# Performance work log

Measured on AMD Instinct MI355X. Metric: run time of the kernel, lower is better.

## Reference

```python
import jax, jax.numpy as jnp
import numpy as np

B, NQ, NV, DIM, HEADS, K = 2, 2048, 2048, 256, 8, 8
HD = DIM // HEADS
HID = 4 * DIM
SCALE = HD ** -0.5
EPS = 1e-5


def setup_inputs() -> dict:
    key = jax.random.key(0)
    ks = jax.random.split(key, 40)
    r = lambda i, s: jax.random.normal(ks[i], s, jnp.float32) * 0.02
    inp = {
        'q': jax.random.normal(ks[0], (B, NQ, DIM), jnp.float32),
        'v': jax.random.normal(ks[1], (B, NV, DIM), jnp.float32),
        'q_pos': jax.random.normal(ks[2], (B, NQ, 3), jnp.float32),
        'v_pos': jax.random.normal(ks[3], (B, NV, 3), jnp.float32),
        'self_knn_index': jax.random.randint(ks[4], (B, NQ, K), 0, NQ, jnp.int32),
        'cross_knn_index': jax.random.randint(ks[5], (B, NQ, K), 0, NV, jnp.int32),
        # LayerNorms (gamma=1, beta=0)
        'norm1_g': jnp.ones(DIM), 'norm1_b': jnp.zeros(DIM),
        'normq_g': jnp.ones(DIM), 'normq_b': jnp.zeros(DIM),
        'normv_g': jnp.ones(DIM), 'normv_b': jnp.zeros(DIM),
        'norm2_g': jnp.ones(DIM), 'norm2_b': jnp.zeros(DIM),
        # self-attention (qkv_bias=False), proj has bias
        'sa_qkv_w': r(6, (DIM, 3 * DIM)),
        'sa_proj_w': r(7, (DIM, DIM)), 'sa_proj_b': jnp.zeros(DIM),
        # cross-attention: q proj and kv proj (no bias), out proj with bias
        'ca_q_w': r(8, (DIM, DIM)),
        'ca_kv_w': r(9, (DIM, 2 * DIM)),
        'ca_proj_w': r(10, (DIM, DIM)), 'ca_proj_b': jnp.zeros(DIM),
        # MLP
        'fc1_w': r(11, (DIM, HID)), 'fc1_b': jnp.zeros(HID),
        'fc2_w': r(12, (HID, DIM)), 'fc2_b': jnp.zeros(DIM),
        # kNN maps
        'knn_w': r(13, (2 * DIM, DIM)), 'knn_b': jnp.zeros(DIM),
        'merge_w': r(14, (2 * DIM, DIM)), 'merge_b': jnp.zeros(DIM),
        'knnx_w': r(15, (2 * DIM, DIM)), 'knnx_b': jnp.zeros(DIM),
        'mergex_w': r(16, (2 * DIM, DIM)), 'mergex_b': jnp.zeros(DIM),
    }
    return inp


def _ln(x, g, b):
    m = x.mean(-1, keepdims=True)
    var = x.var(-1, keepdims=True)
    return (x - m) / jnp.sqrt(var + EPS) * g + b


def _heads(x):  # [B,N,DIM] -> [B,H,N,HD]
    Bx, N, _ = x.shape
    return x.reshape(Bx, N, HEADS, HD).transpose(0, 2, 1, 3)


def _attend(qh, kh, vh, proj_w, proj_b):
    a = jax.nn.softmax(jnp.einsum('bhqd,bhkd->bhqk', qh, kh) * SCALE, axis=-1)
    o = jnp.einsum('bhqk,bhkd->bhqd', a, vh)
    Bx, _, N, _ = o.shape
    o = o.transpose(0, 2, 1, 3).reshape(Bx, N, DIM)
    return o @ proj_w + proj_b


_gather = jax.vmap(lambda pts, idx: pts[idx])  # ([N,D],[Nq,K]) -> [Nq,K,D]


def _knn_feature(qn, vn, idx):  # gather -> diff/cat -> [B,Nq,K,2D]
    local = _gather(vn, idx)                      # [B,Nq,K,D]
    qe = qn[:, :, None, :]                        # [B,Nq,1,D]
    return jnp.concatenate([local - qe, jnp.broadcast_to(qe, local.shape)], -1)


def reference(q, v, q_pos, v_pos, self_knn_index, cross_knn_index,
              norm1_g, norm1_b, normq_g, normq_b, normv_g, normv_b,
              norm2_g, norm2_b, sa_qkv_w, sa_proj_w, sa_proj_b,
              ca_q_w, ca_kv_w, ca_proj_w, ca_proj_b,
              fc1_w, fc1_b, fc2_w, fc2_b,
              knn_w, knn_b, merge_w, merge_b,
              knnx_w, knnx_b, mergex_w, mergex_b):
    # ---- self-attention block with self-kNN branch ----
    nq = _ln(q, norm1_g, norm1_b)
    qkv = nq @ sa_qkv_w
    qh, kh, vh = (_heads(t) for t in jnp.split(qkv, 3, axis=-1))
    sa_out = _attend(qh, kh, vh, sa_proj_w, sa_proj_b)
    f = _knn_feature(nq, nq, self_knn_index)
    knn_out = jax.nn.leaky_relu(f @ knn_w + knn_b, 0.2).max(axis=-2)
    q1 = jnp.concatenate([sa_out, knn_out], -1) @ merge_w + merge_b
    q = q + q1
    # ---- cross-attention block with cross-kNN branch ----
    nq2 = _ln(q, normq_g, normq_b)
    nv = _ln(v, normv_g, normv_b)
    qh = _heads(nq2 @ ca_q_w)
    kh, vh = (_heads(t) for t in jnp.split(nv @ ca_kv_w, 2, axis=-1))
    ca_out = _attend(qh, kh, vh, ca_proj_w, ca_proj_b)
    f = _knn_feature(nq2, nv, cross_knn_index)
    knnx_out = jax.nn.leaky_relu(f @ knnx_w + knnx_b, 0.2).max(axis=-2)
    q2 = jnp.concatenate([ca_out, knnx_out], -1) @ mergex_w + mergex_b
    q = q + q2
    # ---- MLP block ----
    h = _ln(q, norm2_g, norm2_b)
    h = jax.nn.gelu(h @ fc1_w + fc1_b, approximate=False)
    q = q + (h @ fc2_w + fc2_b)
    return q
```

## Files before the change

kernel.cpp:

```cpp
#include <hip/hip_runtime.h>
#include <math.h>

#define NQC   2048
#define NKVC  2048
#define DIMC  256
#define SCALEF 0.17677669529663687f

typedef short bfrag __attribute__((ext_vector_type(8)));
typedef float ffrag __attribute__((ext_vector_type(4)));
typedef unsigned short us8 __attribute__((ext_vector_type(8)));

__device__ __forceinline__ float gelu_exact(float x) {
    return 0.5f * x * (1.0f + erff(x * 0.70710678118654752f));
}
__device__ __forceinline__ unsigned short f2bf(float f) {
    union { float f; unsigned u; } v; v.f = f;
    unsigned r = v.u + 0x7FFFu + ((v.u >> 16) & 1u);
    return (unsigned short)(r >> 16);
}
__device__ __forceinline__ float bf2f(unsigned short u) {
    union { unsigned u; float f; } v; v.u = ((unsigned)u) << 16;
    return v.f;
}

__device__ __forceinline__ void ln_row(
    const float* __restrict__ x, const float* __restrict__ g,
    const float* __restrict__ b, unsigned short* __restrict__ y, int row)
{
    int lane = threadIdx.x & 63;
    const float* xr = x + (size_t)row * DIMC + lane * 4;
    float4 vv = *(const float4*)xr;
    float s  = vv.x + vv.y + vv.z + vv.w;
    float sq = vv.x*vv.x + vv.y*vv.y + vv.z*vv.z + vv.w*vv.w;
    #pragma unroll
    for (int off = 32; off >= 1; off >>= 1) {
        s  += __shfl_xor(s, off);
        sq += __shfl_xor(sq, off);
    }
    float mean = s * (1.0f/DIMC);
    float inv  = rsqrtf(sq * (1.0f/DIMC) - mean*mean + 1e-5f);
    float4 gg = *(const float4*)(g + lane*4);
    float4 bb = *(const float4*)(b + lane*4);
    ushort4 o;
    o.x = f2bf((vv.x - mean) * inv * gg.x + bb.x);
    o.y = f2bf((vv.y - mean) * inv * gg.y + bb.y);
    o.z = f2bf((vv.z - mean) * inv * gg.z + bb.z);
    o.w = f2bf((vv.w - mean) * inv * gg.w + bb.w);
    *(ushort4*)(y + (size_t)row * DIMC + lane * 4) = o;
}

__global__ __launch_bounds__(256) void prep_ln(
    const float* __restrict__ qkv, const float* __restrict__ knn,
    const float* __restrict__ proj, const float* __restrict__ merge,
    const float* __restrict__ caq, const float* __restrict__ knnx,
    const float* __restrict__ cakv, const float* __restrict__ projx,
    const float* __restrict__ mergex, const float* __restrict__ fc1,
    const float* __restrict__ fc2, unsigned short* __restrict__ dst,
    const float* __restrict__ lx, const float* __restrict__ lg,
    const float* __restrict__ lb, unsigned short* __restrict__ ly)
{
    if (blockIdx.x >= 1536) {
        int row = (blockIdx.x - 1536) * 4 + (threadIdx.x >> 6);
        ln_row(lx, lg, lb, ly, row);
        return;
    }
    int e = (blockIdx.x * 256 + threadIdx.x) * 4;
    float v[4];
    float scale = 1.0f;
    if (e < 327680) {
        int n = e >> 8, k = e & 255;
        if (n < 768) {
            const float* s = qkv + (size_t)k * 768 + n;
            #pragma unroll
            for (int i = 0; i < 4; ++i) v[i] = s[(size_t)i * 768];
            if (n < 256) scale = SCALEF;
        } else if (n < 1024) {
            const float* s = knn + (size_t)k * 256 + (n - 768);
            #pragma unroll
            for (int i = 0; i < 4; ++i) v[i] = s[(size_t)i * 256];
        } else {
            const float* s = knn + (size_t)k * 256 + (n - 1024);
            #pragma unroll
            for (int i = 0; i < 4; ++i) v[i] = s[65536 + (size_t)i * 256] - s[(size_t)i * 256];
        }
    } else if (e < 393216) {
        int l = e - 327680, n = l >> 8, k = l & 255;
        const float* s = proj + (size_t)k * 256 + n;
        #pragma unroll
        for (int i = 0; i < 4; ++i) v[i] = s[(size_t)i * 256];
    } else if (e < 524288) {
        int l = e - 393216, n = l >> 9, k = l & 511;
        const float* s = merge + (size_t)k * 256 + n;
        #pragma unroll
        for (int i = 0; i < 4; ++i) v[i] = s[(size_t)i * 256];
    } else if (e < 655360) {
        int l = e - 524288, n = l >> 8, k = l & 255;
        if (n < 256) {
            const float* s = caq + (size_t)k * 256 + n;
            #pragma unroll
            for (int i = 0; i < 4; ++i) v[i] = s[(size_t)i * 256];
            scale = SCALEF;
        } else {
            const float* s = knnx + (size_t)k * 256 + (n - 256);
            #pragma unroll
            for (int i = 0; i < 4; ++i) v[i] = s[65536 + (size_t)i * 256] - s[(size_t)i * 256];
        }
    } else if (e < 851968) {
        int l = e - 655360, n = l >> 8, k = l & 255;
        if (n < 512) {
            const float* s = cakv + (size_t)k * 512 + n;
            #pragma unroll
            for (int i = 0; i < 4; ++i) v[i] = s[(size_t)i * 512];
        } else {
            const float* s = knnx + (size_t)k * 256 + (n - 512);
            #pragma unroll
            for (int i = 0; i < 4; ++i) v[i] = s[(size_t)i * 256];
        }
    } else if (e < 917504) {
        int l = e - 851968, n = l >> 8, k = l & 255;
        const float* s = projx + (size_t)k * 256 + n;
        #pragma unroll
        for (int i = 0; i < 4; ++i) v[i] = s[(size_t)i * 256];
    } else if (e < 1048576) {
        int l = e - 917504, n = l >> 9, k = l & 511;
        const float* s = mergex + (size_t)k * 256 + n;
        #pragma unroll
        for (int i = 0; i < 4; ++i) v[i] = s[(size_t)i * 256];
    } else if (e < 1310720) {
        int l = e - 1048576, n = l >> 8, k = l & 255;
        const float* s = fc1 + (size_t)k * 1024 + n;
        #pragma unroll
        for (int i = 0; i < 4; ++i) v[i] = s[(size_t)i * 1024];
    } else {
        int l = e - 1310720, n = l >> 10, k = l & 1023;
        const float* s = fc2 + (size_t)k * 256 + n;
        #pragma unroll
        for (int i = 0; i < 4; ++i) v[i] = s[(size_t)i * 256];
    }
    ushort4 o;
    o.x = f2bf(v[0] * scale); o.y = f2bf(v[1] * scale);
    o.z = f2bf(v[2] * scale); o.w = f2bf(v[3] * scale);
    *(ushort4*)(dst + e) = o;
}

__global__ __launch_bounds__(256) void ln2_b(
    const float* __restrict__ x1, const float* __restrict__ g1,
    const float* __restrict__ b1, unsigned short* __restrict__ y1,
    const float* __restrict__ x2, const float* __restrict__ g2,
    const float* __restrict__ b2, unsigned short* __restrict__ y2)
{
    int wid = threadIdx.x >> 6;
    int blk = blockIdx.x;
    if (blk < 1024) ln_row(x1, g1, b1, y1, blk * 4 + wid);
    else            ln_row(x2, g2, b2, y2, (blk - 1024) * 4 + wid);
}

__global__ __launch_bounds__(256) void ln_b(
    const float* __restrict__ x, const float* __restrict__ g,
    const float* __restrict__ b, unsigned short* __restrict__ y)
{
    ln_row(x, g, b, y, blockIdx.x * 4 + (threadIdx.x >> 6));
}

template<int ACT, int RESID, int OUTBF>
__global__ __launch_bounds__(256) void gemm64(
    const unsigned short* __restrict__ A, int lda,
    const unsigned short* __restrict__ Wt,
    const float* __restrict__ bias,
    const float* __restrict__ resid, int ldr,
    void* __restrict__ Cp, int ldc, int Kc)
{
    __shared__ unsigned short Alds[64][72];
    __shared__ unsigned short Wlds[64][72];
    const int tid = threadIdx.x;
    const int wid = tid >> 6, lane = tid & 63;
    const int lm = lane & 15, quad = lane >> 4;
    const int wr = wid >> 1, wc = wid & 1;
    const int row0 = blockIdx.y * 64, col0 = blockIdx.x * 64;
    const int ar = tid >> 2, ac = (tid & 3) * 16;
    const unsigned short* Ag = A  + (size_t)(row0 + ar) * lda + ac;
    const unsigned short* Wg = Wt + (size_t)(col0 + ar) * Kc  + ac;

    us8 a0 = *(const us8*)Ag;
    us8 a1 = *(const us8*)(Ag + 8);
    us8 w0 = *(const us8*)Wg;
    us8 w1 = *(const us8*)(Wg + 8);

    ffrag acc[2][2];
    #pragma unroll
    for (int mi = 0; mi < 2; ++mi)
        #pragma unroll
        for (int ni = 0; ni < 2; ++ni)
            acc[mi][ni] = (ffrag){0.f, 0.f, 0.f, 0.f};

    for (int k0 = 0;;) {
        __syncthreads();
        *(us8*)&Alds[ar][ac]   = a0;
        *(us8*)&Alds[ar][ac+8] = a1;
        *(us8*)&Wlds[ar][ac]   = w0;
        *(us8*)&Wlds[ar][ac+8] = w1;
        __syncthreads();
        k0 += 64;
        if (k0 < Kc) {
            a0 = *(const us8*)(Ag + k0);
            a1 = *(const us8*)(Ag + k0 + 8);
            w0 = *(const us8*)(Wg + k0);
            w1 = *(const us8*)(Wg + k0 + 8);
        }
        #pragma unroll
        for (int kc = 0; kc < 2; ++kc) {
            bfrag af[2], bw[2];
            #pragma unroll
            for (int mi = 0; mi < 2; ++mi)
                af[mi] = *(const bfrag*)&Alds[wr*32 + mi*16 + lm][kc*32 + quad*8];
            #pragma unroll
            for (int ni = 0; ni < 2; ++ni)
                bw[ni] = *(const bfrag*)&Wlds[wc*32 + ni*16 + lm][kc*32 + quad*8];
            #pragma unroll
            for (int mi = 0; mi < 2; ++mi)
                #pragma unroll
                for (int ni = 0; ni < 2; ++ni)
                    acc[mi][ni] = __builtin_amdgcn_mfma_f32_16x16x32_bf16(
                        af[mi], bw[ni], acc[mi][ni], 0, 0, 0);
        }
        if (k0 >= Kc) break;
    }
    #pragma unroll
    for (int mi = 0; mi < 2; ++mi) {
        #pragma unroll
        for (int ni = 0; ni < 2; ++ni) {
            int gr = row0 + wr*32 + mi*16 + quad*4;
            int gc = col0 + wc*32 + ni*16 + lm;
            float bv = bias ? bias[gc] : 0.f;
            #pragma unroll
            for (int r = 0; r < 4; ++r) {
                float o = acc[mi][ni][r] + bv;
                if (ACT == 1) o = gelu_exact(o);
                if (RESID) o += resid[(size_t)(gr + r) * ldr + gc];
                if (OUTBF) ((unsigned short*)Cp)[(size_t)(gr + r) * ldc + gc] = f2bf(o);
                else       ((float*)Cp)[(size_t)(gr + r) * ldc + gc] = o;
            }
        }
    }
}

template<int ACT, int RESID, int OUTBF>
__global__ __launch_bounds__(512) void gemm64x8(
    const unsigned short* __restrict__ A, int lda,
    const unsigned short* __restrict__ Wt,
    const float* __restrict__ bias,
    const float* __restrict__ resid, int ldr,
    void* __restrict__ Cp, int ldc, int Kc)
{
    __shared__ unsigned short Alds[2][64][72];
    __shared__ unsigned short Wlds[2][64][72];
    __shared__ float Red[64][68];
    const int tid = threadIdx.x;
    const int g = tid >> 8;
    const int t = tid & 255;
    const int wid2 = (tid >> 6) & 3, lane = tid & 63;
    const int lm = lane & 15, quad = lane >> 4;
    const int wr = wid2 >> 1, wc = wid2 & 1;
    const int row0 = blockIdx.y * 64, col0 = blockIdx.x * 64;
    const int ar = t >> 2, ac = (t & 3) * 16;
    const int KH = Kc >> 1;
    const unsigned short* Ag = A  + (size_t)(row0 + ar) * lda + g * KH + ac;
    const unsigned short* Wg = Wt + (size_t)(col0 + ar) * Kc  + g * KH + ac;

    us8 a0 = *(const us8*)Ag;
    us8 a1 = *(const us8*)(Ag + 8);
    us8 w0 = *(const us8*)Wg;
    us8 w1 = *(const us8*)(Wg + 8);

    ffrag acc[2][2];
    #pragma unroll
    for (int mi = 0; mi < 2; ++mi)
        #pragma unroll
        for (int ni = 0; ni < 2; ++ni)
            acc[mi][ni] = (ffrag){0.f, 0.f, 0.f, 0.f};

    for (int k0 = 0;;) {
        __syncthreads();
        *(us8*)&Alds[g][ar][ac]   = a0;
        *(us8*)&Alds[g][ar][ac+8] = a1;
        *(us8*)&Wlds[g][ar][ac]   = w0;
        *(us8*)&Wlds[g][ar][ac+8] = w1;
        __syncthreads();
        k0 += 64;
        if (k0 < KH) {
            a0 = *(const us8*)(Ag + k0);
            a1 = *(const us8*)(Ag + k0 + 8);
            w0 = *(const us8*)(Wg + k0);
            w1 = *(const us8*)(Wg + k0 + 8);
        }
        #pragma unroll
        for (int kc = 0; kc < 2; ++kc) {
            bfrag af[2], bw[2];
            #pragma unroll
            for (int mi = 0; mi < 2; ++mi)
                af[mi] = *(const bfrag*)&Alds[g][wr*32 + mi*16 + lm][kc*32 + quad*8];
            #pragma unroll
            for (int ni = 0; ni < 2; ++ni)
                bw[ni] = *(const bfrag*)&Wlds[g][wc*32 + ni*16 + lm][kc*32 + quad*8];
            #pragma unroll
            for (int mi = 0; mi < 2; ++mi)
                #pragma unroll
                for (int ni = 0; ni < 2; ++ni)
                    acc[mi][ni] = __builtin_amdgcn_mfma_f32_16x16x32_bf16(
                        af[mi], bw[ni], acc[mi][ni], 0, 0, 0);
        }
        if (k0 >= KH) break;
    }
    __syncthreads();
    if (g == 1) {
        #pragma unroll
        for (int mi = 0; mi < 2; ++mi)
            #pragma unroll
            for (int ni = 0; ni < 2; ++ni) {
                int lr = wr*32 + mi*16 + quad*4;
                int lc = wc*32 + ni*16 + lm;
                #pragma unroll
                for (int r = 0; r < 4; ++r)
                    Red[lr + r][lc] = acc[mi][ni][r];
            }
    }
    __syncthreads();
    if (g == 0) {
        #pragma unroll
        for (int mi = 0; mi < 2; ++mi) {
            #pragma unroll
            for (int ni = 0; ni < 2; ++ni) {
                int lr = wr*32 + mi*16 + quad*4;
                int lc = wc*32 + ni*16 + lm;
                int gr = row0 + lr;
                int gc = col0 + lc;
                float bv = bias ? bias[gc] : 0.f;
                #pragma unroll
                for (int r = 0; r < 4; ++r) {
                    float o = acc[mi][ni][r] + Red[lr + r][lc] + bv;
                    if (ACT == 1) o = gelu_exact(o);
                    if (RESID) o += resid[(size_t)(gr + r) * ldr + gc];
                    if (OUTBF) ((unsigned short*)Cp)[(size_t)(gr + r) * ldc + gc] = f2bf(o);
                    else       ((float*)Cp)[(size_t)(gr + r) * ldc + gc] = o;
                }
            }
        }
    }
}

__global__ __launch_bounds__(256) void gemm64_dual(
    const unsigned short* __restrict__ XB,
    const unsigned short* __restrict__ NVB,
    const unsigned short* __restrict__ WT2,
    const unsigned short* __restrict__ WT3,
    unsigned short* __restrict__ A2,
    unsigned short* __restrict__ A3)
{
    const unsigned short* A; const unsigned short* Wt;
    unsigned short* C; int ldc, col0;
    if (blockIdx.x < 8) { A = XB;  Wt = WT2; C = A2; ldc = 512; col0 = blockIdx.x * 64; }
    else                { A = NVB; Wt = WT3; C = A3; ldc = 768; col0 = (blockIdx.x - 8) * 64; }

    __shared__ unsigned short Alds[64][72];
    __shared__ unsigned short Wlds[64][72];
    const int tid = threadIdx.x;
    const int wid = tid >> 6, lane = tid & 63;
    const int lm = lane & 15, quad = lane >> 4;
    const int wr = wid >> 1, wc = wid & 1;
    const int row0 = blockIdx.y * 64;
    const int ar = tid >> 2, ac = (tid & 3) * 16;
    const unsigned short* Ag = A  + (size_t)(row0 + ar) * 256 + ac;
    const unsigned short* Wg = Wt + (size_t)(col0 + ar) * 256 + ac;

    us8 a0 = *(const us8*)Ag;
    us8 a1 = *(const us8*)(Ag + 8);
    us8 w0 = *(const us8*)Wg;
    us8 w1 = *(const us8*)(Wg + 8);

    ffrag acc[2][2];
    #pragma unroll
    for (int mi = 0; mi < 2; ++mi)
        #pragma unroll
        for (int ni = 0; ni < 2; ++ni)
            acc[mi][ni] = (ffrag){0.f, 0.f, 0.f, 0.f};

    for (int k0 = 0;;) {
        __syncthreads();
        *(us8*)&Alds[ar][ac]   = a0;
        *(us8*)&Alds[ar][ac+8] = a1;
        *(us8*)&Wlds[ar][ac]   = w0;
        *(us8*)&Wlds[ar][ac+8] = w1;
        __syncthreads();
        k0 += 64;
        if (k0 < 256) {
            a0 = *(const us8*)(Ag + k0);
            a1 = *(const us8*)(Ag + k0 + 8);
            w0 = *(const us8*)(Wg + k0);
            w1 = *(const us8*)(Wg + k0 + 8);
        }
        #pragma unroll
        for (int kc = 0; kc < 2; ++kc) {
            bfrag af[2], bw[2];
            #pragma unroll
            for (int mi = 0; mi < 2; ++mi)
                af[mi] = *(const bfrag*)&Alds[wr*32 + mi*16 + lm][kc*32 + quad*8];
            #pragma unroll
            for (int ni = 0; ni < 2; ++ni)
                bw[ni] = *(const bfrag*)&Wlds[wc*32 + ni*16 + lm][kc*32 + quad*8];
            #pragma unroll
            for (int mi = 0; mi < 2; ++mi)
                #pragma unroll
                for (int ni = 0; ni < 2; ++ni)
                    acc[mi][ni] = __builtin_amdgcn_mfma_f32_16x16x32_bf16(
                        af[mi], bw[ni], acc[mi][ni], 0, 0, 0);
        }
        if (k0 >= 256) break;
    }
    #pragma unroll
    for (int mi = 0; mi < 2; ++mi) {
        #pragma unroll
        for (int ni = 0; ni < 2; ++ni) {
            int gr = row0 + wr*32 + mi*16 + quad*4;
            int gc = col0 + wc*32 + ni*16 + lm;
            #pragma unroll
            for (int r = 0; r < 4; ++r)
                C[(size_t)(gr + r) * ldc + gc] = f2bf(acc[mi][ni][r]);
        }
    }
}

__global__ __launch_bounds__(256) void gemm64_comb(
    const unsigned short* __restrict__ Op, const float* __restrict__ Lp,
    const unsigned short* __restrict__ Wt,
    const float* __restrict__ bias,
    unsigned short* __restrict__ C, int ldc)
{
    __shared__ unsigned short Alds[64][72];
    __shared__ unsigned short Wlds[64][72];
    const int tid = threadIdx.x;
    const int wid = tid >> 6, lane = tid & 63;
    const int lm = lane & 15, quad = lane >> 4;
    const int wr = wid >> 1, wc = wid & 1;
    const int row0 = blockIdx.y * 64, col0 = blockIdx.x * 64;
    const int ar = tid >> 2, ac = (tid & 3) * 16;
    const int grow = row0 + ar;
    const unsigned short* O0 = Op + (size_t)grow * 256 + ac;
    const unsigned short* O1 = Op + (size_t)(4096 + grow) * 256 + ac;
    const float* L0 = Lp + (size_t)grow * 8;
    const float* L1 = Lp + (size_t)(4096 + grow) * 8;
    const unsigned short* Wg = Wt + (size_t)(col0 + ar) * 256 + ac;

    us8 o00 = *(const us8*)O0;
    us8 o01 = *(const us8*)(O0 + 8);
    us8 o10 = *(const us8*)O1;
    us8 o11 = *(const us8*)(O1 + 8);
    float li = 1.0f / (L0[ac >> 5] + L1[ac >> 5]);
    us8 w0 = *(const us8*)Wg;
    us8 w1 = *(const us8*)(Wg + 8);

    ffrag acc[2][2];
    #pragma unroll
    for (int mi = 0; mi < 2; ++mi)
        #pragma unroll
        for (int ni = 0; ni < 2; ++ni)
            acc[mi][ni] = (ffrag){0.f, 0.f, 0.f, 0.f};

    for (int k0 = 0;;) {
        us8 ac0, ac1;
        #pragma unroll
        for (int i = 0; i < 8; ++i) {
            ac0[i] = f2bf((bf2f(o00[i]) + bf2f(o10[i])) * li);
            ac1[i] = f2bf((bf2f(o01[i]) + bf2f(o11[i])) * li);
        }
        __syncthreads();
        *(us8*)&Alds[ar][ac]   = ac0;
        *(us8*)&Alds[ar][ac+8] = ac1;
        *(us8*)&Wlds[ar][ac]   = w0;
        *(us8*)&Wlds[ar][ac+8] = w1;
        __syncthreads();
        k0 += 64;
        if (k0 < 256) {
            o00 = *(const us8*)(O0 + k0);
            o01 = *(const us8*)(O0 + k0 + 8);
            o10 = *(const us8*)(O1 + k0);
            o11 = *(const us8*)(O1 + k0 + 8);
            li = 1.0f / (L0[(k0 + ac) >> 5] + L1[(k0 + ac) >> 5]);
            w0 = *(const us8*)(Wg + k0);
            w1 = *(const us8*)(Wg + k0 + 8);
        }
        #pragma unroll
        for (int kc = 0; kc < 2; ++kc) {
            bfrag af[2], bw[2];
            #pragma unroll
            for (int mi = 0; mi < 2; ++mi)
                af[mi] = *(const bfrag*)&Alds[wr*32 + mi*16 + lm][kc*32 + quad*8];
            #pragma unroll
            for (int ni = 0; ni < 2; ++ni)
                bw[ni] = *(const bfrag*)&Wlds[wc*32 + ni*16 + lm][kc*32 + quad*8];
            #pragma unroll
            for (int mi = 0; mi < 2; ++mi)
                #pragma unroll
                for (int ni = 0; ni < 2; ++ni)
                    acc[mi][ni] = __builtin_amdgcn_mfma_f32_16x16x32_bf16(
                        af[mi], bw[ni], acc[mi][ni], 0, 0, 0);
        }
        if (k0 >= 256) break;
    }
    #pragma unroll
    for (int mi = 0; mi < 2; ++mi) {
        #pragma unroll
        for (int ni = 0; ni < 2; ++ni) {
            int gr = row0 + wr*32 + mi*16 + quad*4;
            int gc = col0 + wc*32 + ni*16 + lm;
            float bv = bias[gc];
            #pragma unroll
            for (int r = 0; r < 4; ++r)
                C[(size_t)(gr + r) * ldc + gc] = f2bf(acc[mi][ni][r] + bv);
        }
    }
}

__global__ __launch_bounds__(256) void attn_gather(
    const unsigned short* __restrict__ Qp, int ldq,
    const unsigned short* __restrict__ Kp, int ldk,
    const unsigned short* __restrict__ Vp, int ldv,
    unsigned short* __restrict__ Op, float* __restrict__ Lp,
    const unsigned short* __restrict__ P, int ldp,
    const unsigned short* __restrict__ Base, int ldb,
    const float* __restrict__ gbias, const int* __restrict__ idx,
    unsigned short* __restrict__ gout, int ldgo)
{
    __shared__ unsigned short Klds[64][40];
    __shared__ unsigned short Vt[32][72];
    __shared__ unsigned short Plds[4][16][72];
    int tid = threadIdx.x, wid = tid >> 6, lane = tid & 63;

    if (blockIdx.z >= 4) {
        int gbid = blockIdx.x + 32 * (blockIdx.y + 8 * (blockIdx.z - 4));
        int q = gbid * 4 + wid;
        int b = q >> 11;
        int c = lane * 4;
        ushort4 bu = *(const ushort4*)(Base + (size_t)q * ldb + c);
        float4 bi = *(const float4*)(gbias + c);
        float bsx = bf2f(bu.x) + bi.x, bsy = bf2f(bu.y) + bi.y;
        float bsz = bf2f(bu.z) + bi.z, bsw = bf2f(bu.w) + bi.w;
        float4 acc = make_float4(-3e38f, -3e38f, -3e38f, -3e38f);
        const int* ip = idx + (size_t)q * 8;
        #pragma unroll
        for (int k = 0; k < 8; ++k) {
            int j = ip[k];
            ushort4 pu = *(const ushort4*)(P + ((size_t)(b * NKVC + j)) * ldp + c);
            float t;
            t = bsx + bf2f(pu.x); t = t > 0.f ? t : 0.2f * t; acc.x = fmaxf(acc.x, t);
            t = bsy + bf2f(pu.y); t = t > 0.f ? t : 0.2f * t; acc.y = fmaxf(acc.y, t);
            t = bsz + bf2f(pu.z); t = t > 0.f ? t : 0.2f * t; acc.z = fmaxf(acc.z, t);
            t = bsw + bf2f(pu.w); t = t > 0.f ? t : 0.2f * t; acc.w = fmaxf(acc.w, t);
        }
        ushort4 o;
        o.x = f2bf(acc.x); o.y = f2bf(acc.y); o.z = f2bf(acc.z); o.w = f2bf(acc.w);
        *(ushort4*)(gout + (size_t)q * ldgo + c) = o;
        return;
    }

    int zc = blockIdx.z, bb = zc >> 1, ck = zc & 1;
    int h = blockIdx.y;
    int hoff = h * 32;
    int lm = lane & 15, quad = lane >> 4;
    size_t qbase  = (size_t)bb * NQC;
    size_t kvbase = (size_t)bb * NKVC;
    int q0 = blockIdx.x * 64 + wid * 16;

    bfrag aq = *(const bfrag*)(Qp + (qbase + q0 + lm) * (size_t)ldq + hoff + quad * 8);

    float l_r[4] = {0.f, 0.f, 0.f, 0.f};
    ffrag oacc[2];
    oacc[0] = (ffrag){0.f, 0.f, 0.f, 0.f};
    oacc[1] = (ffrag){0.f, 0.f, 0.f, 0.f};

    const int kkey = tid >> 2, kd0 = (tid & 3) * 8;
    const int vkey = tid & 63, vd0 = (tid >> 6) * 8;
    const unsigned short* kg0 = Kp + (kvbase + kkey) * (size_t)ldk + hoff + kd0;
    const unsigned short* vg0 = Vp + (kvbase + vkey) * (size_t)ldv + hoff + vd0;

    for (int kt = ck * 16; kt < ck * 16 + 16; ++kt) {
        us8 kv = *(const us8*)(kg0 + (size_t)kt * 64 * ldk);
        us8 vv = *(const us8*)(vg0 + (size_t)kt * 64 * ldv);
        __syncthreads();
        *(us8*)&Klds[kkey][kd0] = kv;
        #pragma unroll
        for (int i = 0; i < 8; ++i) Vt[vd0 + i][vkey] = vv[i];
        __syncthreads();

        ffrag sacc[4];
        #pragma unroll
        for (int t = 0; t < 4; ++t) {
            bfrag bk = *(const bfrag*)&Klds[t*16 + lm][quad * 8];
            sacc[t] = __builtin_amdgcn_mfma_f32_16x16x32_bf16(
                aq, bk, (ffrag){0.f,0.f,0.f,0.f}, 0, 0, 0);
        }

        #pragma unroll
        for (int r = 0; r < 4; ++r) {
            float p0 = __expf(sacc[0][r]), p1 = __expf(sacc[1][r]);
            float p2 = __expf(sacc[2][r]), p3 = __expf(sacc[3][r]);
            l_r[r] += (p0 + p1) + (p2 + p3);
            int row = quad * 4 + r;
            Plds[wid][row][lm +  0] = f2bf(p0);
            Plds[wid][row][lm + 16] = f2bf(p1);
            Plds[wid][row][lm + 32] = f2bf(p2);
            Plds[wid][row][lm + 48] = f2bf(p3);
        }
        asm volatile("s_waitcnt lgkmcnt(0)" ::: "memory");

        #pragma unroll
        for (int kc = 0; kc < 2; ++kc) {
            bfrag ap = *(const bfrag*)&Plds[wid][lm][kc*32 + quad*8];
            #pragma unroll
            for (int nt = 0; nt < 2; ++nt) {
                bfrag bv = *(const bfrag*)&Vt[nt*16 + lm][kc*32 + quad*8];
                oacc[nt] = __builtin_amdgcn_mfma_f32_16x16x32_bf16(
                    ap, bv, oacc[nt], 0, 0, 0);
            }
        }
    }
    #pragma unroll
    for (int nt = 0; nt < 2; ++nt)
        #pragma unroll
        for (int r = 0; r < 4; ++r)
            Op[((size_t)ck * 4096 + qbase + q0 + quad*4 + r) * 256 + hoff + nt*16 + lm]
                = f2bf(oacc[nt][r]);
    #pragma unroll
    for (int r = 0; r < 4; ++r) {
        float l = l_r[r];
        l += __shfl_xor(l, 1);
        l += __shfl_xor(l, 2);
        l += __shfl_xor(l, 4);
        l += __shfl_xor(l, 8);
        if (lm == 0)
            Lp[((size_t)ck * 4096 + qbase + q0 + quad*4 + r) * 8 + h] = l;
    }
}

extern "C" void kernel_launch(void* const* d_in, const int* in_sizes, int n_in,
                              void* d_out, int out_size, void* d_ws, size_t ws_size,
                              hipStream_t stream) {
    const float* q_in   = (const float*)d_in[0];
    const float* v_in   = (const float*)d_in[1];
    const int*   idx_s  = (const int*)d_in[4];
    const int*   idx_x  = (const int*)d_in[5];
    const float* n1g = (const float*)d_in[6],  *n1b = (const float*)d_in[7];
    const float* nqg = (const float*)d_in[8],  *nqb = (const float*)d_in[9];
    const float* nvg = (const float*)d_in[10], *nvb = (const float*)d_in[11];
    const float* n2g = (const float*)d_in[12], *n2b = (const float*)d_in[13];
    const float* sa_qkv_w  = (const float*)d_in[14];
    const float* sa_proj_w = (const float*)d_in[15];
    const float* sa_proj_b = (const float*)d_in[16];
    const float* ca_q_w    = (const float*)d_in[17];
    const float* ca_kv_w   = (const float*)d_in[18];
    const float* ca_proj_w = (const float*)d_in[19];
    const float* ca_proj_b = (const float*)d_in[20];
    const float* fc1_w = (const float*)d_in[21], *fc1_b = (const float*)d_in[22];
    const float* fc2_w = (const float*)d_in[23], *fc2_b = (const float*)d_in[24];
    const float* knn_w   = (const float*)d_in[25], *knn_b   = (const float*)d_in[26];
    const float* merge_w = (const float*)d_in[27], *merge_b = (const float*)d_in[28];
    const float* knnx_w  = (const float*)d_in[29], *knnx_b  = (const float*)d_in[30];
    const float* mergex_w = (const float*)d_in[31], *mergex_b = (const float*)d_in[32];
    float* out = (float*)d_out;

    unsigned short* A1      = (unsigned short*)d_ws;
    unsigned short* A2      = A1;
    unsigned short* A3      = A1 + (size_t)4096 * 512;
    unsigned short* Hb      = A1;
    unsigned short* KN      = A1 + (size_t)4096 * 1280;
    unsigned short* CC      = KN;
    unsigned short* XB      = CC + (size_t)4096 * 512;
    unsigned short* NVB     = XB + (size_t)4096 * 256;
    unsigned short* WT      = NVB + (size_t)4096 * 256;
    unsigned short* WT1     = WT;
    unsigned short* WTproj  = WT + 327680;
    unsigned short* WTmerge = WT + 393216;
    unsigned short* WT2     = WT + 524288;
    unsigned short* WT3     = WT + 655360;
    unsigned short* WTprojx = WT + 851968;
    unsigned short* WTmergex= WT + 917504;
    unsigned short* WTfc1   = WT + 1048576;
    unsigned short* WTfc2   = WT + 1310720;
    unsigned short* Opart   = WT + 1572864;
    float* Lpart = (float*)(Opart + (size_t)2 * 4096 * 256);

    dim3 blk(256), blk8(512);
    dim3 gAG(NQC / 64, 8, 8);

    prep_ln<<<dim3(2560), blk, 0, stream>>>(sa_qkv_w, knn_w, sa_proj_w, merge_w,
        ca_q_w, knnx_w, ca_kv_w, ca_proj_w, mergex_w, fc1_w, fc2_w, WT,
        q_in, n1g, n1b, XB);

    gemm64<0,0,1><<<dim3(20,64), blk, 0, stream>>>(XB, 256, WT1,
        nullptr, nullptr, 0, A1, 1280, 256);
    attn_gather<<<gAG, blk, 0, stream>>>(A1, 1280, A1+256, 1280, A1+512, 1280,
        Opart, Lpart, A1+768, 1280, A1+1024, 1280, knn_b, idx_s, CC+256, 512);
    gemm64_comb<<<dim3(4,64), blk, 0, stream>>>(Opart, Lpart, WTproj,
        sa_proj_b, CC, 512);
    gemm64x8<0,1,0><<<dim3(4,64), blk8, 0, stream>>>(CC, 512, WTmerge,
        merge_b, q_in, 256, out, 256, 512);

    ln2_b<<<dim3(2048), blk, 0, stream>>>(out, nqg, nqb, XB,
        v_in, nvg, nvb, NVB);
    gemm64_dual<<<dim3(20,64), blk, 0, stream>>>(XB, NVB, WT2, WT3, A2, A3);
    attn_gather<<<gAG, blk, 0, stream>>>(A2, 512, A3, 768, A3+256, 768,
        Opart, Lpart, A3+512, 768, A2+256, 512, knnx_b, idx_x, CC+256, 512);
    gemm64_comb<<<dim3(4,64), blk, 0, stream>>>(Opart, Lpart, WTprojx,
        ca_proj_b, CC, 512);
    gemm64x8<0,1,0><<<dim3(4,64), blk8, 0, stream>>>(CC, 512, WTmergex,
        mergex_b, out, 256, out, 256, 512);

    ln_b<<<dim3(1024), blk, 0, stream>>>(out, n2g, n2b, XB);
    gemm64<1,0,1><<<dim3(16,64), blk, 0, stream>>>(XB, 256, WTfc1,
        fc1_b, nullptr, 0, Hb, 1024, 256);
    gemm64x8<0,1,0><<<dim3(4,64), blk8, 0, stream>>>(Hb, 1024, WTfc2,
        fc2_b, out, 256, out, 256, 1024);
}
```

Before: 258.9 us.

## Fold attention output projection into merge weights and fuse combine with merge GEMM

Precomputes the product of proj_w and the attention half of merge_w, plus a folded bias, inside the prep and QKV kernels. The separate combine/proj GEMM and merge GEMM are replaced by one split-K kernel that normalises the partial attention outputs and multiplies them and the kNN branch concurrently. The v LayerNorm moves into the prep kernel. Softmax switches to a raw exp2 with log2e folded into the scale, and P is packed with a bf16 pack instruction through a permuted V layout. Intermediate rounding changes: the folded weights are rounded to bf16 and the attention output skips a rounding step.

```diff
diff --git a/kernel.cpp b/kernel.cpp
--- a/kernel.cpp
+++ b/kernel.cpp
@@ -4,7 +4,7 @@
 #define NQC   2048
 #define NKVC  2048
 #define DIMC  256
-#define SCALEF 0.17677669529663687f
+#define SCALEF 0.2550348810731232f
 
 typedef short bfrag __attribute__((ext_vector_type(8)));
 typedef float ffrag __attribute__((ext_vector_type(4)));
@@ -21,6 +21,13 @@
 __device__ __forceinline__ float bf2f(unsigned short u) {
     union { unsigned u; float f; } v; v.u = ((unsigned)u) << 16;
     return v.f;
+}
+__device__ __forceinline__ float fexp2(float x) {
+    float r; asm("v_exp_f32 %0, %1" : "=v"(r) : "v"(x)); return r;
+}
+__device__ __forceinline__ unsigned cvt_pk_bf16(float lo, float hi) {
+    unsigned r; asm("v_cvt_pk_bf16_f32 %0, %1, %2" : "=v"(r) : "v"(lo), "v"(hi));
+    return r;
 }
 
 __device__ __forceinline__ void ln_row(
@@ -57,8 +64,28 @@
     const float* __restrict__ mergex, const float* __restrict__ fc1,
     const float* __restrict__ fc2, unsigned short* __restrict__ dst,
     const float* __restrict__ lx, const float* __restrict__ lg,
-    const float* __restrict__ lb, unsigned short* __restrict__ ly)
-{
+    const float* __restrict__ lb, unsigned short* __restrict__ ly,
+    const float* __restrict__ vx, const float* __restrict__ vg,
+    const float* __restrict__ vb, unsigned short* __restrict__ vy,
+    const float* __restrict__ pb1, const float* __restrict__ mb1, float* __restrict__ bf1o,
+    const float* __restrict__ pbx, const float* __restrict__ mbx, float* __restrict__ bfxo)
+{
+    if (blockIdx.x >= 3584) {
+        const float* bp = (blockIdx.x == 3584) ? pb1 : pbx;
+        const float* Wm = (blockIdx.x == 3584) ? merge : mergex;
+        const float* bm = (blockIdx.x == 3584) ? mb1 : mbx;
+        float* o        = (blockIdx.x == 3584) ? bf1o : bfxo;
+        int m = threadIdx.x;
+        float acc = bm[m];
+        for (int k = 0; k < 256; ++k) acc += bp[k] * Wm[(size_t)k * 256 + m];
+        o[m] = acc;
+        return;
+    }
+    if (blockIdx.x >= 2560) {
+        int row = (blockIdx.x - 2560) * 4 + (threadIdx.x >> 6);
+        ln_row(vx, vg, vb, vy, row);
+        return;
+    }
     if (blockIdx.x >= 1536) {
         int row = (blockIdx.x - 1536) * 4 + (threadIdx.x >> 6);
         ln_row(lx, lg, lb, ly, row);
@@ -84,10 +111,10 @@
             for (int i = 0; i < 4; ++i) v[i] = s[65536 + (size_t)i * 256] - s[(size_t)i * 256];
         }
     } else if (e < 393216) {
-        int l = e - 327680, n = l >> 8, k = l & 255;
-        const float* s = proj + (size_t)k * 256 + n;
-        #pragma unroll
-        for (int i = 0; i < 4; ++i) v[i] = s[(size_t)i * 256];
+        int l = e - 327680;
+        const float* s = proj + l;
+        #pragma unroll
+        for (int i = 0; i < 4; ++i) v[i] = s[i];
     } else if (e < 524288) {
         int l = e - 393216, n = l >> 9, k = l & 511;
         const float* s = merge + (size_t)k * 256 + n;
@@ -117,10 +144,10 @@
             for (int i = 0; i < 4; ++i) v[i] = s[(size_t)i * 256];
         }
     } else if (e < 917504) {
-        int l = e - 851968, n = l >> 8, k = l & 255;
-        const float* s = projx + (size_t)k * 256 + n;
-        #pragma unroll
-        for (int i = 0; i < 4; ++i) v[i] = s[(size_t)i * 256];
+        int l = e - 851968;
+        const float* s = projx + l;
+        #pragma unroll
+        for (int i = 0; i < 4; ++i) v[i] = s[i];
     } else if (e < 1048576) {
         int l = e - 917504, n = l >> 9, k = l & 511;
         const float* s = mergex + (size_t)k * 256 + n;
@@ -143,18 +170,6 @@
     *(ushort4*)(dst + e) = o;
 }
 
-__global__ __launch_bounds__(256) void ln2_b(
-    const float* __restrict__ x1, const float* __restrict__ g1,
-    const float* __restrict__ b1, unsigned short* __restrict__ y1,
-    const float* __restrict__ x2, const float* __restrict__ g2,
-    const float* __restrict__ b2, unsigned short* __restrict__ y2)
-{
-    int wid = threadIdx.x >> 6;
-    int blk = blockIdx.x;
-    if (blk < 1024) ln_row(x1, g1, b1, y1, blk * 4 + wid);
-    else            ln_row(x2, g2, b2, y2, (blk - 1024) * 4 + wid);
-}
-
 __global__ __launch_bounds__(256) void ln_b(
     const float* __restrict__ x, const float* __restrict__ g,
     const float* __restrict__ b, unsigned short* __restrict__ y)
@@ -163,20 +178,19 @@
 }
 
 template<int ACT, int RESID, int OUTBF>
-__global__ __launch_bounds__(256) void gemm64(
+__device__ __forceinline__ void gemm_body(
     const unsigned short* __restrict__ A, int lda,
     const unsigned short* __restrict__ Wt,
     const float* __restrict__ bias,
     const float* __restrict__ resid, int ldr,
-    void* __restrict__ Cp, int ldc, int Kc)
-{
-    __shared__ unsigned short Alds[64][72];
-    __shared__ unsigned short Wlds[64][72];
+    void* __restrict__ Cp, int ldc, int Kc, int row0, int col0,
+    unsigned short (* __restrict__ Alds)[72],
+    unsigned short (* __restrict__ Wlds)[72])
+{
     const int tid = threadIdx.x;
     const int wid = tid >> 6, lane = tid & 63;
     const int lm = lane & 15, quad = lane >> 4;
     const int wr = wid >> 1, wc = wid & 1;
-    const int row0 = blockIdx.y * 64, col0 = blockIdx.x * 64;
     const int ar = tid >> 2, ac = (tid & 3) * 16;
     const unsigned short* Ag = A  + (size_t)(row0 + ar) * lda + ac;
     const unsigned short* Wg = Wt + (size_t)(col0 + ar) * Kc  + ac;
@@ -242,6 +256,45 @@
             }
         }
     }
+}
+
+template<int ACT, int RESID, int OUTBF>
+__global__ __launch_bounds__(256) void gemm64(
+    const unsigned short* __restrict__ A, int lda,
+    const unsigned short* __restrict__ Wt,
+    const float* __restrict__ bias,
+    const float* __restrict__ resid, int ldr,
+    void* __restrict__ Cp, int ldc, int Kc)
+{
+    __shared__ unsigned short Alds[64][72];
+    __shared__ unsigned short Wlds[64][72];
+    gemm_body<ACT,RESID,OUTBF>(A, lda, Wt, bias, resid, ldr, Cp, ldc, Kc,
+                               blockIdx.y * 64, blockIdx.x * 64, Alds, Wlds);
+}
+
+__global__ __launch_bounds__(256) void gemm_qkv_fold(
+    const unsigned short* __restrict__ XB, const unsigned short* __restrict__ WT1,
+    unsigned short* __restrict__ A1,
+    const unsigned short* __restrict__ WTmerge, const unsigned short* __restrict__ projbf,
+    unsigned short* __restrict__ WTf1,
+    const unsigned short* __restrict__ WTmergex, const unsigned short* __restrict__ projxbf,
+    unsigned short* __restrict__ WTfx)
+{
+    __shared__ unsigned short Alds[64][72];
+    __shared__ unsigned short Wlds[64][72];
+    const unsigned short *A, *Wt; unsigned short* C;
+    int lda, ldc, row0, col0;
+    if (blockIdx.y >= 64) {
+        if (blockIdx.x >= 16) return;
+        row0 = (blockIdx.x >> 2) * 64; col0 = (blockIdx.x & 3) * 64;
+        lda = 512; ldc = 256;
+        if (blockIdx.y == 64) { A = WTmerge;  Wt = projbf;  C = WTf1; }
+        else                  { A = WTmergex; Wt = projxbf; C = WTfx; }
+    } else {
+        A = XB; Wt = WT1; C = A1; lda = 256; ldc = 1280;
+        row0 = blockIdx.y * 64; col0 = blockIdx.x * 64;
+    }
+    gemm_body<0,0,1>(A, lda, Wt, nullptr, nullptr, 0, C, ldc, 256, row0, col0, Alds, Wlds);
 }
 
 template<int ACT, int RESID, int OUTBF>
@@ -348,6 +401,134 @@
     }
 }
 
+__global__ __launch_bounds__(512) void gemm64x8f(
+    const unsigned short* __restrict__ Op, const float* __restrict__ Lp,
+    const unsigned short* __restrict__ Akn,
+    const unsigned short* __restrict__ Wat,
+    const unsigned short* __restrict__ Wkn,
+    const float* __restrict__ bias,
+    const float* __restrict__ resid,
+    float* __restrict__ Cp)
+{
+    __shared__ unsigned short Alds[2][64][72];
+    __shared__ unsigned short Wlds[2][64][72];
+    __shared__ float Red[64][68];
+    const int tid = threadIdx.x;
+    const int g = tid >> 8;
+    const int t = tid & 255;
+    const int wid2 = (tid >> 6) & 3, lane = tid & 63;
+    const int lm = lane & 15, quad = lane >> 4;
+    const int wr = wid2 >> 1, wc = wid2 & 1;
+    const int row0 = blockIdx.y * 64, col0 = blockIdx.x * 64;
+    const int ar = t >> 2, ac = (t & 3) * 16;
+    const int grow = row0 + ar;
+
+    const unsigned short* O0 = Op + (size_t)grow * 256 + ac;
+    const unsigned short* O1 = Op + (size_t)(4096 + grow) * 256 + ac;
+    const float* L0 = Lp + (size_t)grow * 8;
+    const float* L1 = Lp + (size_t)(4096 + grow) * 8;
+    const unsigned short* Ak = Akn + (size_t)grow * 512 + ac;
+    const unsigned short* Wg = g ? Wkn + (size_t)(col0 + ar) * 512 + ac
+                                 : Wat + (size_t)(col0 + ar) * 256 + ac;
+
+    us8 a0, a1, o10, o11;
+    float li = 0.f;
+    if (g == 0) {
+        a0  = *(const us8*)O0;  a1  = *(const us8*)(O0 + 8);
+        o10 = *(const us8*)O1;  o11 = *(const us8*)(O1 + 8);
+        li  = 1.0f / (L0[ac >> 5] + L1[ac >> 5]);
+    } else {
+        a0 = *(const us8*)Ak;   a1 = *(const us8*)(Ak + 8);
+    }
+    us8 w0 = *(const us8*)Wg;
+    us8 w1 = *(const us8*)(Wg + 8);
+
+    ffrag acc[2][2];
+    #pragma unroll
+    for (int mi = 0; mi < 2; ++mi)
+        #pragma unroll
+        for (int ni = 0; ni < 2; ++ni)
+            acc[mi][ni] = (ffrag){0.f, 0.f, 0.f, 0.f};
+
+    for (int k0 = 0;;) {
+        us8 s0 = a0, s1 = a1;
+        if (g == 0) {
+            #pragma unroll
+            for (int i = 0; i < 8; ++i) {
+                s0[i] = f2bf((bf2f(a0[i]) + bf2f(o10[i])) * li);
+                s1[i] = f2bf((bf2f(a1[i]) + bf2f(o11[i])) * li);
+            }
+        }
+        __syncthreads();
+        *(us8*)&Alds[g][ar][ac]   = s0;
+        *(us8*)&Alds[g][ar][ac+8] = s1;
+        *(us8*)&Wlds[g][ar][ac]   = w0;
+        *(us8*)&Wlds[g][ar][ac+8] = w1;
+        __syncthreads();
+        k0 += 64;
+        if (k0 < 256) {
+            if (g == 0) {
+                a0  = *(const us8*)(O0 + k0);  a1  = *(const us8*)(O0 + k0 + 8);
+                o10 = *(const us8*)(O1 + k0);  o11 = *(const us8*)(O1 + k0 + 8);
+                li  = 1.0f / (L0[(k0 + ac) >> 5] + L1[(k0 + ac) >> 5]);
+            } else {
+                a0 = *(const us8*)(Ak + k0);   a1 = *(const us8*)(Ak + k0 + 8);
+            }
+            w0 = *(const us8*)(Wg + k0);
+            w1 = *(const us8*)(Wg + k0 + 8);
+        }
+        #pragma unroll
+        for (int kc = 0; kc < 2; ++kc) {
+            bfrag af[2], bw[2];
+            #pragma unroll
+            for (int mi = 0; mi < 2; ++mi)
+                af[mi] = *(const bfrag*)&Alds[g][wr*32 + mi*16 + lm][kc*32 + quad*8];
+            #pragma unroll
+            for (int ni = 0; ni < 2; ++ni)
+                bw[ni] = *(const bfrag*)&Wlds[g][wc*32 + ni*16 + lm][kc*32 + quad*8];
+            #pragma unroll
+            for (int mi = 0; mi < 2; ++mi)
+                #pragma unroll
+                for (int ni = 0; ni < 2; ++ni)
+                    acc[mi][ni] = __builtin_amdgcn_mfma_f32_16x16x32_bf16(
+                        af[mi], bw[ni], acc[mi][ni], 0, 0, 0);
+        }
+        if (k0 >= 256) break;
+    }
+    __syncthreads();
+    if (g == 1) {
+        #pragma unroll
+        for (int mi = 0; mi < 2; ++mi)
+            #pragma unroll
+            for (int ni = 0; ni < 2; ++ni) {
+                int lr = wr*32 + mi*16 + quad*4;
+                int lc = wc*32 + ni*16 + lm;
+                #pragma unroll
+                for (int r = 0; r < 4; ++r)
+                    Red[lr + r][lc] = acc[mi][ni][r];
+            }
+    }
+    __syncthreads();
+    if (g == 0) {
+        #pragma unroll
+        for (int mi = 0; mi < 2; ++mi) {
+            #pragma unroll
+            for (int ni = 0; ni < 2; ++ni) {
+                int lr = wr*32 + mi*16 + quad*4;
+                int lc = wc*32 + ni*16 + lm;
+                int gr = row0 + lr;
+                int gc = col0 + lc;
+                float bv = bias[gc];
+                #pragma unroll
+                for (int r = 0; r < 4; ++r)
+                    Cp[(size_t)(gr + r) * 256 + gc] =
+                        acc[mi][ni][r] + Red[lr + r][lc] + bv
+                        + resid[(size_t)(gr + r) * 256 + gc];
+            }
+        }
+    }
+}
+
 __global__ __launch_bounds__(256) void gemm64_dual(
     const unsigned short* __restrict__ XB,
     const unsigned short* __restrict__ NVB,
@@ -356,168 +537,14 @@
     unsigned short* __restrict__ A2,
     unsigned short* __restrict__ A3)
 {
+    __shared__ unsigned short Alds[64][72];
+    __shared__ unsigned short Wlds[64][72];
     const unsigned short* A; const unsigned short* Wt;
     unsigned short* C; int ldc, col0;
     if (blockIdx.x < 8) { A = XB;  Wt = WT2; C = A2; ldc = 512; col0 = blockIdx.x * 64; }
     else                { A = NVB; Wt = WT3; C = A3; ldc = 768; col0 = (blockIdx.x - 8) * 64; }
-
-    __shared__ unsigned short Alds[64][72];
-    __shared__ unsigned short Wlds[64][72];
-    const int tid = threadIdx.x;
-    const int wid = tid >> 6, lane = tid & 63;
-    const int lm = lane & 15, quad = lane >> 4;
-    const int wr = wid >> 1, wc = wid & 1;
-    const int row0 = blockIdx.y * 64;
-    const int ar = tid >> 2, ac = (tid & 3) * 16;
-    const unsigned short* Ag = A  + (size_t)(row0 + ar) * 256 + ac;
-    const unsigned short* Wg = Wt + (size_t)(col0 + ar) * 256 + ac;
-
-    us8 a0 = *(const us8*)Ag;
-    us8 a1 = *(const us8*)(Ag + 8);
-    us8 w0 = *(const us8*)Wg;
-    us8 w1 = *(const us8*)(Wg + 8);
-
-    ffrag acc[2][2];
-    #pragma unroll
-    for (int mi = 0; mi < 2; ++mi)
-        #pragma unroll
-        for (int ni = 0; ni < 2; ++ni)
-            acc[mi][ni] = (ffrag){0.f, 0.f, 0.f, 0.f};
-
-    for (int k0 = 0;;) {
-        __syncthreads();
-        *(us8*)&Alds[ar][ac]   = a0;
-        *(us8*)&Alds[ar][ac+8] = a1;
-        *(us8*)&Wlds[ar][ac]   = w0;
-        *(us8*)&Wlds[ar][ac+8] = w1;
-        __syncthreads();
-        k0 += 64;
-        if (k0 < 256) {
-            a0 = *(const us8*)(Ag + k0);
-            a1 = *(const us8*)(Ag + k0 + 8);
-            w0 = *(const us8*)(Wg + k0);
-            w1 = *(const us8*)(Wg + k0 + 8);
-        }
-        #pragma unroll
-        for (int kc = 0; kc < 2; ++kc) {
-            bfrag af[2], bw[2];
-            #pragma unroll
-            for (int mi = 0; mi < 2; ++mi)
-                af[mi] = *(const bfrag*)&Alds[wr*32 + mi*16 + lm][kc*32 + quad*8];
-            #pragma unroll
-            for (int ni = 0; ni < 2; ++ni)
-                bw[ni] = *(const bfrag*)&Wlds[wc*32 + ni*16 + lm][kc*32 + quad*8];
-            #pragma unroll
-            for (int mi = 0; mi < 2; ++mi)
-                #pragma unroll
-                for (int ni = 0; ni < 2; ++ni)
-                    acc[mi][ni] = __builtin_amdgcn_mfma_f32_16x16x32_bf16(
-                        af[mi], bw[ni], acc[mi][ni], 0, 0, 0);
-        }
-        if (k0 >= 256) break;
-    }
-    #pragma unroll
-    for (int mi = 0; mi < 2; ++mi) {
-        #pragma unroll
-        for (int ni = 0; ni < 2; ++ni) {
-            int gr = row0 + wr*32 + mi*16 + quad*4;
-            int gc = col0 + wc*32 + ni*16 + lm;
-            #pragma unroll
-            for (int r = 0; r < 4; ++r)
-                C[(size_t)(gr + r) * ldc + gc] = f2bf(acc[mi][ni][r]);
-        }
-    }
-}
-
-__global__ __launch_bounds__(256) void gemm64_comb(
-    const unsigned short* __restrict__ Op, const float* __restrict__ Lp,
-    const unsigned short* __restrict__ Wt,
-    const float* __restrict__ bias,
-    unsigned short* __restrict__ C, int ldc)
-{
-    __shared__ unsigned short Alds[64][72];
-    __shared__ unsigned short Wlds[64][72];
-    const int tid = threadIdx.x;
-    const int wid = tid >> 6, lane = tid & 63;
-    const int lm = lane & 15, quad = lane >> 4;
-    const int wr = wid >> 1, wc = wid & 1;
-    const int row0 = blockIdx.y * 64, col0 = blockIdx.x * 64;
-    const int ar = tid >> 2, ac = (tid & 3) * 16;
-    const int grow = row0 + ar;
-    const unsigned short* O0 = Op + (size_t)grow * 256 + ac;
-    const unsigned short* O1 = Op + (size_t)(4096 + grow) * 256 + ac;
-    const float* L0 = Lp + (size_t)grow * 8;
-    const float* L1 = Lp + (size_t)(4096 + grow) * 8;
-    const unsigned short* Wg = Wt + (size_t)(col0 + ar) * 256 + ac;
-
-    us8 o00 = *(const us8*)O0;
-    us8 o01 = *(const us8*)(O0 + 8);
-    us8 o10 = *(const us8*)O1;
-    us8 o11 = *(const us8*)(O1 + 8);
-    float li = 1.0f / (L0[ac >> 5] + L1[ac >> 5]);
-    us8 w0 = *(const us8*)Wg;
-    us8 w1 = *(const us8*)(Wg + 8);
-
-    ffrag acc[2][2];
-    #pragma unroll
-    for (int mi = 0; mi < 2; ++mi)
-        #pragma unroll
-        for (int ni = 0; ni < 2; ++ni)
-            acc[mi][ni] = (ffrag){0.f, 0.f, 0.f, 0.f};
-
-    for (int k0 = 0;;) {
-        us8 ac0, ac1;
-        #pragma unroll
-        for (int i = 0; i < 8; ++i) {
-            ac0[i] = f2bf((bf2f(o00[i]) + bf2f(o10[i])) * li);
-            ac1[i] = f2bf((bf2f(o01[i]) + bf2f(o11[i])) * li);
-        }
-        __syncthreads();
-        *(us8*)&Alds[ar][ac]   = ac0;
-        *(us8*)&Alds[ar][ac+8] = ac1;
-        *(us8*)&Wlds[ar][ac]   = w0;
-        *(us8*)&Wlds[ar][ac+8] = w1;
-        __syncthreads();
-        k0 += 64;
-        if (k0 < 256) {
-            o00 = *(const us8*)(O0 + k0);
-            o01 = *(const us8*)(O0 + k0 + 8);
-            o10 = *(const us8*)(O1 + k0);
-            o11 = *(const us8*)(O1 + k0 + 8);
-            li = 1.0f / (L0[(k0 + ac) >> 5] + L1[(k0 + ac) >> 5]);
-            w0 = *(const us8*)(Wg + k0);
-            w1 = *(const us8*)(Wg + k0 + 8);
-        }
-        #pragma unroll
-        for (int kc = 0; kc < 2; ++kc) {
-            bfrag af[2], bw[2];
-            #pragma unroll
-            for (int mi = 0; mi < 2; ++mi)
-                af[mi] = *(const bfrag*)&Alds[wr*32 + mi*16 + lm][kc*32 + quad*8];
-            #pragma unroll
-            for (int ni = 0; ni < 2; ++ni)
-                bw[ni] = *(const bfrag*)&Wlds[wc*32 + ni*16 + lm][kc*32 + quad*8];
-            #pragma unroll
-            for (int mi = 0; mi < 2; ++mi)
-                #pragma unroll
-                for (int ni = 0; ni < 2; ++ni)
-                    acc[mi][ni] = __builtin_amdgcn_mfma_f32_16x16x32_bf16(
-                        af[mi], bw[ni], acc[mi][ni], 0, 0, 0);
-        }
-        if (k0 >= 256) break;
-    }
-    #pragma unroll
-    for (int mi = 0; mi < 2; ++mi) {
-        #pragma unroll
-        for (int ni = 0; ni < 2; ++ni) {
-            int gr = row0 + wr*32 + mi*16 + quad*4;
-            int gc = col0 + wc*32 + ni*16 + lm;
-            float bv = bias[gc];
-            #pragma unroll
-            for (int r = 0; r < 4; ++r)
-                C[(size_t)(gr + r) * ldc + gc] = f2bf(acc[mi][ni][r] + bv);
-        }
-    }
+    gemm_body<0,0,1>(A, 256, Wt, nullptr, nullptr, 0, C, ldc, 256,
+                     blockIdx.y * 64, col0, Alds, Wlds);
 }
 
 __global__ __launch_bounds__(256) void attn_gather(
@@ -531,8 +558,8 @@
     unsigned short* __restrict__ gout, int ldgo)
 {
     __shared__ unsigned short Klds[64][40];
-    __shared__ unsigned short Vt[32][72];
-    __shared__ unsigned short Plds[4][16][72];
+    __shared__ __align__(16) unsigned short Vt[32][72];
+    __shared__ __align__(16) unsigned short Plds[4][16][72];
     int tid = threadIdx.x, wid = tid >> 6, lane = tid & 63;
 
     if (blockIdx.z >= 4) {
@@ -579,6 +606,7 @@
 
     const int kkey = tid >> 2, kd0 = (tid & 3) * 8;
     const int vkey = tid & 63, vd0 = (tid >> 6) * 8;
+    const int vcol = ((vkey & 15) << 2) | (vkey >> 4);
     const unsigned short* kg0 = Kp + (kvbase + kkey) * (size_t)ldk + hoff + kd0;
     const unsigned short* vg0 = Vp + (kvbase + vkey) * (size_t)ldv + hoff + vd0;
 
@@ -588,7 +616,7 @@
         __syncthreads();
         *(us8*)&Klds[kkey][kd0] = kv;
         #pragma unroll
-        for (int i = 0; i < 8; ++i) Vt[vd0 + i][vkey] = vv[i];
+        for (int i = 0; i < 8; ++i) Vt[vd0 + i][vcol] = vv[i];
         __syncthreads();
 
         ffrag sacc[4];
@@ -601,14 +629,12 @@
 
         #pragma unroll
         for (int r = 0; r < 4; ++r) {
-            float p0 = __expf(sacc[0][r]), p1 = __expf(sacc[1][r]);
-            float p2 = __expf(sacc[2][r]), p3 = __expf(sacc[3][r]);
+            float p0 = fexp2(sacc[0][r]), p1 = fexp2(sacc[1][r]);
+            float p2 = fexp2(sacc[2][r]), p3 = fexp2(sacc[3][r]);
             l_r[r] += (p0 + p1) + (p2 + p3);
-            int row = quad * 4 + r;
-            Plds[wid][row][lm +  0] = f2bf(p0);
-            Plds[wid][row][lm + 16] = f2bf(p1);
-            Plds[wid][row][lm + 32] = f2bf(p2);
-            Plds[wid][row][lm + 48] = f2bf(p3);
+            unsigned u0 = cvt_pk_bf16(p0, p1);
+            unsigned u1 = cvt_pk_bf16(p2, p3);
+            *(uint2*)&Plds[wid][quad*4 + r][lm << 2] = make_uint2(u0, u1);
         }
         asm volatile("s_waitcnt lgkmcnt(0)" ::: "memory");
 
@@ -677,42 +703,44 @@
     unsigned short* NVB     = XB + (size_t)4096 * 256;
     unsigned short* WT      = NVB + (size_t)4096 * 256;
     unsigned short* WT1     = WT;
-    unsigned short* WTproj  = WT + 327680;
+    unsigned short* projbf  = WT + 327680;
     unsigned short* WTmerge = WT + 393216;
     unsigned short* WT2     = WT + 524288;
     unsigned short* WT3     = WT + 655360;
-    unsigned short* WTprojx = WT + 851968;
+    unsigned short* projxbf = WT + 851968;
     unsigned short* WTmergex= WT + 917504;
     unsigned short* WTfc1   = WT + 1048576;
     unsigned short* WTfc2   = WT + 1310720;
     unsigned short* Opart   = WT + 1572864;
     float* Lpart = (float*)(Opart + (size_t)2 * 4096 * 256);
+    unsigned short* WTf1 = (unsigned short*)(Lpart + (size_t)2 * 4096 * 8);
+    unsigned short* WTfx = WTf1 + 65536;
+    float* bf1 = (float*)(WTfx + 65536);
+    float* bfx = bf1 + 256;
 
     dim3 blk(256), blk8(512);
     dim3 gAG(NQC / 64, 8, 8);
 
-    prep_ln<<<dim3(2560), blk, 0, stream>>>(sa_qkv_w, knn_w, sa_proj_w, merge_w,
+    prep_ln<<<dim3(3586), blk, 0, stream>>>(sa_qkv_w, knn_w, sa_proj_w, merge_w,
         ca_q_w, knnx_w, ca_kv_w, ca_proj_w, mergex_w, fc1_w, fc2_w, WT,
-        q_in, n1g, n1b, XB);
-
-    gemm64<0,0,1><<<dim3(20,64), blk, 0, stream>>>(XB, 256, WT1,
-        nullptr, nullptr, 0, A1, 1280, 256);
+        q_in, n1g, n1b, XB,
+        v_in, nvg, nvb, NVB,
+        sa_proj_b, merge_b, bf1,
+        ca_proj_b, mergex_b, bfx);
+
+    gemm_qkv_fold<<<dim3(20,66), blk, 0, stream>>>(XB, WT1, A1,
+        WTmerge, projbf, WTf1, WTmergex, projxbf, WTfx);
     attn_gather<<<gAG, blk, 0, stream>>>(A1, 1280, A1+256, 1280, A1+512, 1280,
         Opart, Lpart, A1+768, 1280, A1+1024, 1280, knn_b, idx_s, CC+256, 512);
-    gemm64_comb<<<dim3(4,64), blk, 0, stream>>>(Opart, Lpart, WTproj,
-        sa_proj_b, CC, 512);
-    gemm64x8<0,1,0><<<dim3(4,64), blk8, 0, stream>>>(CC, 512, WTmerge,
-        merge_b, q_in, 256, out, 256, 512);
-
-    ln2_b<<<dim3(2048), blk, 0, stream>>>(out, nqg, nqb, XB,
-        v_in, nvg, nvb, NVB);
+    gemm64x8f<<<dim3(4,64), blk8, 0, stream>>>(Opart, Lpart, CC+256,
+        WTf1, WTmerge+256, bf1, q_in, out);
+
+    ln_b<<<dim3(1024), blk, 0, stream>>>(out, nqg, nqb, XB);
     gemm64_dual<<<dim3(20,64), blk, 0, stream>>>(XB, NVB, WT2, WT3, A2, A3);
     attn_gather<<<gAG, blk, 0, stream>>>(A2, 512, A3, 768, A3+256, 768,
         Opart, Lpart, A3+512, 768, A2+256, 512, knnx_b, idx_x, CC+256, 512);
-    gemm64_comb<<<dim3(4,64), blk, 0, stream>>>(Opart, Lpart, WTprojx,
-        ca_proj_b, CC, 512);
-    gemm64x8<0,1,0><<<dim3(4,64), blk8, 0, stream>>>(CC, 512, WTmergex,
-        mergex_b, out, 256, out, 256, 512);
+    gemm64x8f<<<dim3(4,64), blk8, 0, stream>>>(Opart, Lpart, CC+256,
+        WTfx, WTmergex+256, bfx, out, out);
 
     ln_b<<<dim3(1024), blk, 0, stream>>>(out, n2g, n2b, XB);
     gemm64<1,0,1><<<dim3(16,64), blk, 0, stream>>>(XB, 256, WTfc1,
```

Result: faster. 245.3 us (-5.3%).
